# Optimization experiments

Measured on AMD Instinct MI355X. Metric: run time of the kernel, lower is better.

The kernel has to match this reference:

```python
import jax, jax.numpy as jnp
import numpy as np

N = 131072   # nodes (flattened batch)
SI, VI = 128, 64   # in_dims
SO, VO = 128, 64   # out_dims
HD = 128           # h_dim


def setup_inputs() -> dict:
    key = jax.random.key(0)
    ks = jax.random.split(key, 8)
    scale = lambda fan_in: 1.0 / np.sqrt(fan_in)
    return {
        "s": jax.random.normal(ks[0], (N, SI), dtype=jnp.float32),
        "V": jax.random.normal(ks[1], (N, VI, 3), dtype=jnp.float32),
        # Linear(vi, h_dim, bias=False): weight [h_dim, vi]
        "W_h": jax.random.uniform(ks[2], (HD, VI), jnp.float32, -scale(VI), scale(VI)),
        # Linear(h_dim, vo, bias=False): weight [vo, h_dim]
        "W_V": jax.random.uniform(ks[3], (VO, HD), jnp.float32, -scale(HD), scale(HD)),
        # Linear(si + h_dim, so)
        "W_s_w": jax.random.uniform(ks[4], (SO, SI + HD), jnp.float32, -scale(SI + HD), scale(SI + HD)),
        "W_s_b": jax.random.uniform(ks[5], (SO,), jnp.float32, -scale(SI + HD), scale(SI + HD)),
        # Linear(so, vo) gate
        "W_g_w": jax.random.uniform(ks[6], (VO, SO), jnp.float32, -scale(SO), scale(SO)),
        "W_g_b": jax.random.uniform(ks[7], (VO,), jnp.float32, -scale(SO), scale(SO)),
    }


def reference(s, V, W_h, W_V, W_s_w, W_s_b, W_g_w, W_g_b):
    # Vh: contract vector-channel dim vi, keep 3 spatial dims -> [N, h_dim, 3]
    Vh = jnp.einsum("nvc,hv->nhc", V, W_h)
    # L2 norm over the 3 spatial dims -> [N, h_dim]
    Vh_norm = jnp.sqrt(jnp.sum(Vh * Vh, axis=-1))
    # V_out: [N, vo, 3]
    V_out = jnp.einsum("nhc,oh->noc", Vh, W_V)
    # scalar path: concat + linear + relu -> [N, so]
    s_cat = jnp.concatenate([s, Vh_norm], axis=-1)
    s_out = jax.nn.relu(s_cat @ W_s_w.T + W_s_b)
    # vector gate: sigmoid(Linear(s_out)) broadcast over spatial dim
    gate = jax.nn.sigmoid(s_out @ W_g_w.T + W_g_b)[..., None]  # [N, vo, 1]
    V_out = V_out * gate
    return s_out, V_out
```

## Files before the change

### kernel.cpp

```cpp
#include <hip/hip_runtime.h>
#include <hip/hip_bf16.h>
#include <math.h>

#define NNODES 131072
#define BN 32

typedef __attribute__((ext_vector_type(8))) short bf16x8;
typedef __attribute__((ext_vector_type(4))) float f32x4;

__device__ short g_w[57344];

__device__ __forceinline__ short f2b(float f) {
  union { float f; unsigned u; } x; x.f = f;
  unsigned r = x.u + 0x7fffu + ((x.u >> 16) & 1u);
  return (short)(r >> 16);
}

__global__ void prep_kernel(const float* __restrict__ W_h, const float* __restrict__ W_V,
                            const float* __restrict__ W_s_w, const float* __restrict__ W_g_w) {
  int i4 = (blockIdx.x * 256 + threadIdx.x) * 4;
  if (i4 >= 57344) return;
  const float* src;
  if (i4 < 8192)       src = W_h   + i4;
  else if (i4 < 16384) src = W_V   + (i4 - 8192);
  else if (i4 < 49152) src = W_s_w + (i4 - 16384);
  else                 src = W_g_w + (i4 - 49152);
  float4 q = *(const float4*)src;
  short4 p;
  p.x = f2b(q.x); p.y = f2b(q.y); p.z = f2b(q.z); p.w = f2b(q.w);
  *(short4*)(g_w + i4) = p;
}


__global__ __launch_bounds__(256, 3)
void gvp_kernel(const float* __restrict__ s_in, const float* __restrict__ V_in,
                const float* __restrict__ W_s_b, const float* __restrict__ W_g_b,
                float* __restrict__ s_out_g, float* __restrict__ V_out_g)
{
  __shared__ __align__(16) char smem[49152];
  char*  const Vt   = smem;
  char*  const VH   = smem;
  float* const VST  = (float*)smem;
  char*  const SC   = smem + 24576;
  float* const GATE = (float*)(smem + 24576);
  char*  const SOUT = smem + 40960;

  const short* const g_wh = g_w;
  const short* const g_wv = g_w + 8192;
  const short* const g_ws = g_w + 16384;
  const short* const g_wg = g_w + 49152;

  const int t    = threadIdx.x;
  const int lane = t & 63;
  const int w    = t >> 6;
  const int l15  = lane & 15;
  const int lk8  = (lane >> 4) << 3;
  const int r4   = (lane >> 4) << 2;
  const long n0  = (long)blockIdx.x * BN;

  {
    const float4* Vb = (const float4*)(V_in + n0 * 192);
    #pragma unroll
    for (int i = 0; i < 6; ++i) {
      int idx = t + 256 * i;
      float4 q = Vb[idx];
      int f = idx << 2;
      #pragma unroll
      for (int e = 0; e < 4; ++e) {
        int ff = f + e;
        int nl = ff / 192;
        int r  = ff - nl * 192;
        int v  = r / 3;
        int c  = r - v * 3;
        int row = (c << 5) + nl;
        unsigned a = (unsigned)(row * 128) + (((unsigned)(v * 2)) ^ (unsigned)((row & 7) << 4));
        *(short*)(Vt + a) = f2b(((const float*)&q)[e]);
      }
    }
  }
  {
    const float4* sb = (const float4*)(s_in + n0 * 128);
    #pragma unroll
    for (int i = 0; i < 4; ++i) {
      int idx = t + 256 * i;
      float4 q = sb[idx];
      int f = idx << 2;
      int nl = f >> 7;
      int k  = f & 127;
      ushort4 p;
      p.x = (unsigned short)f2b(q.x);
      p.y = (unsigned short)f2b(q.y);
      p.z = (unsigned short)f2b(q.z);
      p.w = (unsigned short)f2b(q.w);
      unsigned a = (unsigned)(nl * 512) + (((unsigned)(k * 2)) ^ (unsigned)((nl & 7) << 4));
      *(ushort4*)(SC + a) = p;
    }
  }
  __syncthreads();

  f32x4 acc1[6][2];
  #pragma unroll
  for (int rt = 0; rt < 6; ++rt) {
    f32x4 z = {0.f, 0.f, 0.f, 0.f};
    acc1[rt][0] = z; acc1[rt][1] = z;
  }
  {
    bf16x8 bf1[2][2];
    #pragma unroll
    for (int cc = 0; cc < 2; ++cc) {
      int h = ((2 * w + cc) << 4) + l15;
      #pragma unroll
      for (int ks = 0; ks < 2; ++ks)
        bf1[cc][ks] = *(const bf16x8*)(g_wh + h * 64 + (ks << 5) + lk8);
    }
    #pragma unroll
    for (int rt = 0; rt < 6; ++rt) {
      int row = (rt << 4) + l15;
      unsigned sw = (unsigned)((row & 7) << 4);
      bf16x8 af0 = *(const bf16x8*)(Vt + row * 128 + (((unsigned)(lk8 * 2)) ^ sw));
      bf16x8 af1 = *(const bf16x8*)(Vt + row * 128 + (((unsigned)((32 + lk8) * 2)) ^ sw));
      #pragma unroll
      for (int cc = 0; cc < 2; ++cc) {
        acc1[rt][cc] = __builtin_amdgcn_mfma_f32_16x16x32_bf16(af0, bf1[cc][0], acc1[rt][cc], 0, 0, 0);
        acc1[rt][cc] = __builtin_amdgcn_mfma_f32_16x16x32_bf16(af1, bf1[cc][1], acc1[rt][cc], 0, 0, 0);
      }
    }
  }
  __syncthreads();

  #pragma unroll
  for (int cc = 0; cc < 2; ++cc) {
    int col = ((2 * w + cc) << 4) + l15;
    #pragma unroll
    for (int rt = 0; rt < 6; ++rt) {
      #pragma unroll
      for (int i = 0; i < 4; ++i) {
        int row = (rt << 4) + r4 + i;
        unsigned a = (unsigned)(row * 256) + (((unsigned)(col * 2)) ^ (unsigned)((row & 7) << 4));
        *(short*)(VH + a) = f2b(acc1[rt][cc][i]);
      }
    }
    #pragma unroll
    for (int rt = 0; rt < 2; ++rt) {
      #pragma unroll
      for (int i = 0; i < 4; ++i) {
        int nl = (rt << 4) + r4 + i;
        float x0 = acc1[rt][cc][i];
        float x1 = acc1[rt + 2][cc][i];
        float x2 = acc1[rt + 4][cc][i];
        float nrm = sqrtf(x0 * x0 + x1 * x1 + x2 * x2);
        int k = 128 + col;
        unsigned a = (unsigned)(nl * 512) + (((unsigned)(k * 2)) ^ (unsigned)((nl & 7) << 4));
        *(short*)(SC + a) = f2b(nrm);
      }
    }
  }
  __syncthreads();

  f32x4 acc2[6];
  #pragma unroll
  for (int rt = 0; rt < 6; ++rt) { f32x4 z = {0.f,0.f,0.f,0.f}; acc2[rt] = z; }
  {
    bf16x8 bf2[4];
    int o = (w << 4) + l15;
    #pragma unroll
    for (int ks = 0; ks < 4; ++ks)
      bf2[ks] = *(const bf16x8*)(g_wv + o * 128 + (ks << 5) + lk8);
    #pragma unroll
    for (int rt = 0; rt < 6; ++rt) {
      int row = (rt << 4) + l15;
      unsigned sw = (unsigned)((row & 7) << 4);
      #pragma unroll
      for (int ks = 0; ks < 4; ++ks) {
        bf16x8 a = *(const bf16x8*)(VH + row * 256 + (((unsigned)((((ks << 5) + lk8)) * 2)) ^ sw));
        acc2[rt] = __builtin_amdgcn_mfma_f32_16x16x32_bf16(a, bf2[ks], acc2[rt], 0, 0, 0);
      }
    }
  }

  f32x4 acc3[2][2];
  {
    f32x4 z = {0.f,0.f,0.f,0.f};
    acc3[0][0] = z; acc3[0][1] = z; acc3[1][0] = z; acc3[1][1] = z;
  }
  #pragma unroll
  for (int ks = 0; ks < 8; ++ks) {
    bf16x8 b3[2];
    #pragma unroll
    for (int cc = 0; cc < 2; ++cc) {
      int o = ((w + 4 * cc) << 4) + l15;
      b3[cc] = *(const bf16x8*)(g_ws + o * 256 + (ks << 5) + lk8);
    }
    #pragma unroll
    for (int rt = 0; rt < 2; ++rt) {
      int row = (rt << 4) + l15;
      bf16x8 a = *(const bf16x8*)(SC + row * 512 +
                   (((unsigned)(((ks << 5) + lk8) * 2)) ^ ((unsigned)((row & 7) << 4))));
      acc3[rt][0] = __builtin_amdgcn_mfma_f32_16x16x32_bf16(a, b3[0], acc3[rt][0], 0, 0, 0);
      acc3[rt][1] = __builtin_amdgcn_mfma_f32_16x16x32_bf16(a, b3[1], acc3[rt][1], 0, 0, 0);
    }
  }
  #pragma unroll
  for (int cc = 0; cc < 2; ++cc) {
    int col = ((w + 4 * cc) << 4) + l15;
    float bias = W_s_b[col];
    #pragma unroll
    for (int rt = 0; rt < 2; ++rt) {
      #pragma unroll
      for (int i = 0; i < 4; ++i) {
        int row = (rt << 4) + r4 + i;
        float val = fmaxf(acc3[rt][cc][i] + bias, 0.0f);
        s_out_g[(n0 + row) * 128 + col] = val;
        unsigned a = (unsigned)(row * 256) + (((unsigned)(col * 2)) ^ (unsigned)((row & 7) << 4));
        *(short*)(SOUT + a) = f2b(val);
      }
    }
  }
  __syncthreads();

  f32x4 acc4[2];
  { f32x4 z = {0.f,0.f,0.f,0.f}; acc4[0] = z; acc4[1] = z; }
  {
    int o = (w << 4) + l15;
    #pragma unroll
    for (int ks = 0; ks < 4; ++ks) {
      bf16x8 b4 = *(const bf16x8*)(g_wg + o * 128 + (ks << 5) + lk8);
      #pragma unroll
      for (int rt = 0; rt < 2; ++rt) {
        int row = (rt << 4) + l15;
        bf16x8 a = *(const bf16x8*)(SOUT + row * 256 +
                     (((unsigned)(((ks << 5) + lk8) * 2)) ^ ((unsigned)((row & 7) << 4))));
        acc4[rt] = __builtin_amdgcn_mfma_f32_16x16x32_bf16(a, b4, acc4[rt], 0, 0, 0);
      }
    }
    float bias = W_g_b[o];
    #pragma unroll
    for (int rt = 0; rt < 2; ++rt) {
      #pragma unroll
      for (int i = 0; i < 4; ++i) {
        int nl = (rt << 4) + r4 + i;
        float x = acc4[rt][i] + bias;
        GATE[nl * 64 + o] = 1.0f / (1.0f + __expf(-x));
      }
    }
  }
  __syncthreads();

  {
    int col = (w << 4) + l15;
    #pragma unroll
    for (int rt = 0; rt < 6; ++rt) {
      #pragma unroll
      for (int i = 0; i < 4; ++i) {
        int row = (rt << 4) + r4 + i;
        int c  = row >> 5;
        int nl = row & 31;
        VST[nl * 192 + col * 3 + c] = acc2[rt][i] * GATE[nl * 64 + col];
      }
    }
  }
  __syncthreads();

  {
    float4* Vo = (float4*)(V_out_g + n0 * 192);
    const float4* Vs = (const float4*)VST;
    #pragma unroll
    for (int i = 0; i < 6; ++i) {
      int idx = t + 256 * i;
      Vo[idx] = Vs[idx];
    }
  }
}

extern "C" void kernel_launch(void* const* d_in, const int* in_sizes, int n_in,
                              void* d_out, int out_size, void* d_ws, size_t ws_size,
                              hipStream_t stream) {
  const float* s_in  = (const float*)d_in[0];
  const float* V_in  = (const float*)d_in[1];
  const float* W_h   = (const float*)d_in[2];
  const float* W_V   = (const float*)d_in[3];
  const float* W_s_w = (const float*)d_in[4];
  const float* W_s_b = (const float*)d_in[5];
  const float* W_g_w = (const float*)d_in[6];
  const float* W_g_b = (const float*)d_in[7];
  float* out = (float*)d_out;
  float* s_out_g = out;
  float* V_out_g = out + (size_t)NNODES * 128;
  hipLaunchKernelGGL(prep_kernel, dim3(57344 / (256 * 4)), dim3(256), 0, stream,
                     W_h, W_V, W_s_w, W_g_w);
  hipLaunchKernelGGL(gvp_kernel, dim3(NNODES / BN), dim3(256), 0, stream,
                     s_in, V_in, W_s_b, W_g_b, s_out_g, V_out_g);
}
```

Before: 117.6 us.

## Shrink LDS to 32KB by reading s directly from global and keeping gate in registers

Stops staging the scalar input s in shared memory. The scalar GEMM now loads s straight from global memory and converts it to bf16 in registers for its first half of K, and reads the norm part from a smaller LDS buffer. The gate sigmoid stays in registers and is applied directly to the V_out accumulators, because each wave's gate columns match its V_out columns. This removes the GATE buffer and one barrier, cutting LDS from 48KB to 32KB and raising the launch-bounds occupancy target from 3 to 5. In exchange, s is read from global with uncoalesced 32-byte per-lane accesses inside the MFMA loop, and register pressure rises.

```diff
diff --git a/kernel.cpp b/kernel.cpp
--- a/kernel.cpp
+++ b/kernel.cpp
@@ -14,6 +14,14 @@
   union { float f; unsigned u; } x; x.f = f;
   unsigned r = x.u + 0x7fffu + ((x.u >> 16) & 1u);
   return (short)(r >> 16);
+}
+__device__ __forceinline__ bf16x8 cvt8(const float* __restrict__ p) {
+  float4 qa = *(const float4*)p;
+  float4 qb = *(const float4*)(p + 4);
+  bf16x8 fr;
+  fr[0] = f2b(qa.x); fr[1] = f2b(qa.y); fr[2] = f2b(qa.z); fr[3] = f2b(qa.w);
+  fr[4] = f2b(qb.x); fr[5] = f2b(qb.y); fr[6] = f2b(qb.z); fr[7] = f2b(qb.w);
+  return fr;
 }
 
 __global__ void prep_kernel(const float* __restrict__ W_h, const float* __restrict__ W_V,
@@ -32,18 +40,17 @@
 }
 
 
-__global__ __launch_bounds__(256, 3)
+__global__ __launch_bounds__(256, 5)
 void gvp_kernel(const float* __restrict__ s_in, const float* __restrict__ V_in,
                 const float* __restrict__ W_s_b, const float* __restrict__ W_g_b,
                 float* __restrict__ s_out_g, float* __restrict__ V_out_g)
 {
-  __shared__ __align__(16) char smem[49152];
+  __shared__ __align__(16) char smem[32768];
   char*  const Vt   = smem;
   char*  const VH   = smem;
   float* const VST  = (float*)smem;
-  char*  const SC   = smem + 24576;
-  float* const GATE = (float*)(smem + 24576);
-  char*  const SOUT = smem + 40960;
+  char*  const NORM = smem + 24576;
+  char*  const SOUT = smem + 24576;
 
   const short* const g_wh = g_w;
   const short* const g_wv = g_w + 8192;
@@ -78,24 +85,6 @@
       }
     }
   }
-  {
-    const float4* sb = (const float4*)(s_in + n0 * 128);
-    #pragma unroll
-    for (int i = 0; i < 4; ++i) {
-      int idx = t + 256 * i;
-      float4 q = sb[idx];
-      int f = idx << 2;
-      int nl = f >> 7;
-      int k  = f & 127;
-      ushort4 p;
-      p.x = (unsigned short)f2b(q.x);
-      p.y = (unsigned short)f2b(q.y);
-      p.z = (unsigned short)f2b(q.z);
-      p.w = (unsigned short)f2b(q.w);
-      unsigned a = (unsigned)(nl * 512) + (((unsigned)(k * 2)) ^ (unsigned)((nl & 7) << 4));
-      *(ushort4*)(SC + a) = p;
-    }
-  }
   __syncthreads();
 
   f32x4 acc1[6][2];
@@ -149,9 +138,8 @@
         float x1 = acc1[rt + 2][cc][i];
         float x2 = acc1[rt + 4][cc][i];
         float nrm = sqrtf(x0 * x0 + x1 * x1 + x2 * x2);
-        int k = 128 + col;
-        unsigned a = (unsigned)(nl * 512) + (((unsigned)(k * 2)) ^ (unsigned)((nl & 7) << 4));
-        *(short*)(SC + a) = f2b(nrm);
+        unsigned a = (unsigned)(nl * 256) + (((unsigned)(col * 2)) ^ (unsigned)((nl & 7) << 4));
+        *(short*)(NORM + a) = f2b(nrm);
       }
     }
   }
@@ -194,12 +182,19 @@
     #pragma unroll
     for (int rt = 0; rt < 2; ++rt) {
       int row = (rt << 4) + l15;
-      bf16x8 a = *(const bf16x8*)(SC + row * 512 +
-                   (((unsigned)(((ks << 5) + lk8) * 2)) ^ ((unsigned)((row & 7) << 4))));
+      bf16x8 a;
+      if (ks < 4) {
+        a = cvt8(s_in + (n0 + row) * 128 + (ks << 5) + lk8);
+      } else {
+        a = *(const bf16x8*)(NORM + row * 256 +
+              (((unsigned)((((ks - 4) << 5) + lk8) * 2)) ^ ((unsigned)((row & 7) << 4))));
+      }
       acc3[rt][0] = __builtin_amdgcn_mfma_f32_16x16x32_bf16(a, b3[0], acc3[rt][0], 0, 0, 0);
       acc3[rt][1] = __builtin_amdgcn_mfma_f32_16x16x32_bf16(a, b3[1], acc3[rt][1], 0, 0, 0);
     }
   }
+  __syncthreads();
+
   #pragma unroll
   for (int cc = 0; cc < 2; ++cc) {
     int col = ((w + 4 * cc) << 4) + l15;
@@ -220,6 +215,7 @@
 
   f32x4 acc4[2];
   { f32x4 z = {0.f,0.f,0.f,0.f}; acc4[0] = z; acc4[1] = z; }
+  float sig[2][4];
   {
     int o = (w << 4) + l15;
     #pragma unroll
@@ -235,16 +231,13 @@
     }
     float bias = W_g_b[o];
     #pragma unroll
-    for (int rt = 0; rt < 2; ++rt) {
-      #pragma unroll
-      for (int i = 0; i < 4; ++i) {
-        int nl = (rt << 4) + r4 + i;
+    for (int rt = 0; rt < 2; ++rt)
+      #pragma unroll
+      for (int i = 0; i < 4; ++i) {
         float x = acc4[rt][i] + bias;
-        GATE[nl * 64 + o] = 1.0f / (1.0f + __expf(-x));
-      }
-    }
-  }
-  __syncthreads();
+        sig[rt][i] = 1.0f / (1.0f + __expf(-x));
+      }
+  }
 
   {
     int col = (w << 4) + l15;
@@ -252,10 +245,9 @@
     for (int rt = 0; rt < 6; ++rt) {
       #pragma unroll
       for (int i = 0; i < 4; ++i) {
-        int row = (rt << 4) + r4 + i;
-        int c  = row >> 5;
-        int nl = row & 31;
-        VST[nl * 192 + col * 3 + c] = acc2[rt][i] * GATE[nl * 64 + col];
+        int c  = rt >> 1;
+        int nl = ((rt & 1) << 4) + r4 + i;
+        VST[nl * 192 + col * 3 + c] = acc2[rt][i] * sig[rt & 1][i];
       }
     }
   }
```

Result: slower. 192.5 us (+63.7%).

## Shrink LDS footprint, keep gate in registers, raise occupancy to four blocks

Applied to the files above, without the earlier changes.

Splits the concatenated scalar/norm buffer into two separate 256-byte-stride regions and reuses the norm region for the s_out staging, cutting shared memory from 48KB to 40KB. It then raises the launch bound so four blocks can be resident per CU. The gate values now stay in registers, because the gate GEMM's output layout matches the V_out accumulator layout, which removes the GATE LDS round trip and one barrier. A barrier is added before SOUT overwrites NORM, and the s_out column mapping is changed so each wave owns two adjacent 16-column tiles. The tighter register budget from the higher occupancy target risks spills.

```diff
diff --git a/kernel.cpp b/kernel.cpp
--- a/kernel.cpp
+++ b/kernel.cpp
@@ -32,18 +32,18 @@
 }
 
 
-__global__ __launch_bounds__(256, 3)
+__global__ __launch_bounds__(256, 4)
 void gvp_kernel(const float* __restrict__ s_in, const float* __restrict__ V_in,
                 const float* __restrict__ W_s_b, const float* __restrict__ W_g_b,
                 float* __restrict__ s_out_g, float* __restrict__ V_out_g)
 {
-  __shared__ __align__(16) char smem[49152];
+  __shared__ __align__(16) char smem[40960];
   char*  const Vt   = smem;
   char*  const VH   = smem;
   float* const VST  = (float*)smem;
   char*  const SC   = smem + 24576;
-  float* const GATE = (float*)(smem + 24576);
-  char*  const SOUT = smem + 40960;
+  char*  const NORM = smem + 32768;
+  char*  const SOUT = smem + 32768;
 
   const short* const g_wh = g_w;
   const short* const g_wv = g_w + 8192;
@@ -92,7 +92,7 @@
       p.y = (unsigned short)f2b(q.y);
       p.z = (unsigned short)f2b(q.z);
       p.w = (unsigned short)f2b(q.w);
-      unsigned a = (unsigned)(nl * 512) + (((unsigned)(k * 2)) ^ (unsigned)((nl & 7) << 4));
+      unsigned a = (unsigned)(nl * 256) + (((unsigned)(k * 2)) ^ (unsigned)((nl & 7) << 4));
       *(ushort4*)(SC + a) = p;
     }
   }
@@ -149,9 +149,8 @@
         float x1 = acc1[rt + 2][cc][i];
         float x2 = acc1[rt + 4][cc][i];
         float nrm = sqrtf(x0 * x0 + x1 * x1 + x2 * x2);
-        int k = 128 + col;
-        unsigned a = (unsigned)(nl * 512) + (((unsigned)(k * 2)) ^ (unsigned)((nl & 7) << 4));
-        *(short*)(SC + a) = f2b(nrm);
+        unsigned a = (unsigned)(nl * 256) + (((unsigned)(col * 2)) ^ (unsigned)((nl & 7) << 4));
+        *(short*)(NORM + a) = f2b(nrm);
       }
     }
   }
@@ -188,31 +187,43 @@
     bf16x8 b3[2];
     #pragma unroll
     for (int cc = 0; cc < 2; ++cc) {
-      int o = ((w + 4 * cc) << 4) + l15;
+      int o = (w << 5) + (cc << 4) + l15;
       b3[cc] = *(const bf16x8*)(g_ws + o * 256 + (ks << 5) + lk8);
     }
     #pragma unroll
     for (int rt = 0; rt < 2; ++rt) {
       int row = (rt << 4) + l15;
-      bf16x8 a = *(const bf16x8*)(SC + row * 512 +
-                   (((unsigned)(((ks << 5) + lk8) * 2)) ^ ((unsigned)((row & 7) << 4))));
+      unsigned sw = (unsigned)((row & 7) << 4);
+      bf16x8 a;
+      if (ks < 4) {
+        a = *(const bf16x8*)(SC + row * 256 + (((unsigned)(((ks << 5) + lk8) * 2)) ^ sw));
+      } else {
+        a = *(const bf16x8*)(NORM + row * 256 + (((unsigned)((((ks - 4) << 5) + lk8) * 2)) ^ sw));
+      }
       acc3[rt][0] = __builtin_amdgcn_mfma_f32_16x16x32_bf16(a, b3[0], acc3[rt][0], 0, 0, 0);
       acc3[rt][1] = __builtin_amdgcn_mfma_f32_16x16x32_bf16(a, b3[1], acc3[rt][1], 0, 0, 0);
     }
   }
-  #pragma unroll
-  for (int cc = 0; cc < 2; ++cc) {
-    int col = ((w + 4 * cc) << 4) + l15;
-    float bias = W_s_b[col];
+  __syncthreads();
+
+  {
+    float bias0 = W_s_b[(w << 5) + l15];
+    float bias1 = W_s_b[(w << 5) + 16 + l15];
     #pragma unroll
     for (int rt = 0; rt < 2; ++rt) {
       #pragma unroll
       for (int i = 0; i < 4; ++i) {
         int row = (rt << 4) + r4 + i;
-        float val = fmaxf(acc3[rt][cc][i] + bias, 0.0f);
-        s_out_g[(n0 + row) * 128 + col] = val;
-        unsigned a = (unsigned)(row * 256) + (((unsigned)(col * 2)) ^ (unsigned)((row & 7) << 4));
-        *(short*)(SOUT + a) = f2b(val);
+        unsigned sw = (unsigned)((row & 7) << 4);
+        float v0 = fmaxf(acc3[rt][0][i] + bias0, 0.0f);
+        float v1 = fmaxf(acc3[rt][1][i] + bias1, 0.0f);
+        int col0 = (w << 5) + l15;
+        s_out_g[(n0 + row) * 128 + col0]      = v0;
+        s_out_g[(n0 + row) * 128 + col0 + 16] = v1;
+        unsigned a0 = (unsigned)(row * 256) + (((unsigned)(col0 * 2)) ^ sw);
+        unsigned a1 = (unsigned)(row * 256) + (((unsigned)((col0 + 16) * 2)) ^ sw);
+        *(short*)(SOUT + a0) = f2b(v0);
+        *(short*)(SOUT + a1) = f2b(v1);
       }
     }
   }
@@ -220,6 +231,7 @@
 
   f32x4 acc4[2];
   { f32x4 z = {0.f,0.f,0.f,0.f}; acc4[0] = z; acc4[1] = z; }
+  float sig[2][4];
   {
     int o = (w << 4) + l15;
     #pragma unroll
@@ -235,16 +247,13 @@
     }
     float bias = W_g_b[o];
     #pragma unroll
-    for (int rt = 0; rt < 2; ++rt) {
-      #pragma unroll
-      for (int i = 0; i < 4; ++i) {
-        int nl = (rt << 4) + r4 + i;
+    for (int rt = 0; rt < 2; ++rt)
+      #pragma unroll
+      for (int i = 0; i < 4; ++i) {
         float x = acc4[rt][i] + bias;
-        GATE[nl * 64 + o] = 1.0f / (1.0f + __expf(-x));
-      }
-    }
-  }
-  __syncthreads();
+        sig[rt][i] = 1.0f / (1.0f + __expf(-x));
+      }
+  }
 
   {
     int col = (w << 4) + l15;
@@ -252,10 +261,9 @@
     for (int rt = 0; rt < 6; ++rt) {
       #pragma unroll
       for (int i = 0; i < 4; ++i) {
-        int row = (rt << 4) + r4 + i;
-        int c  = row >> 5;
-        int nl = row & 31;
-        VST[nl * 192 + col * 3 + c] = acc2[rt][i] * GATE[nl * 64 + col];
+        int c  = rt >> 1;
+        int nl = ((rt & 1) << 4) + r4 + i;
+        VST[nl * 192 + col * 3 + c] = acc2[rt][i] * sig[rt & 1][i];
       }
     }
   }
```

After: 120.5 us. 1.03x slower.
